# Optimization experiments

Hardware: AMD Instinct MI355X
Metric: run time of the kernel (lower is better)

Reference implementation:

```python
import jax, jax.numpy as jnp
import numpy as np

N = 50000
E = 800000
B = 8  # number of graphs


def gcn_conv(x, src, dst, W, b, n_nodes):
    # PyG GCNConv: add self-loops, symmetric deg^{-1/2} normalization,
    # linear transform, scatter-add aggregation at dst, then bias.
    loops = jnp.arange(n_nodes, dtype=src.dtype)
    s = jnp.concatenate([src, loops])
    d = jnp.concatenate([dst, loops])
    deg = jax.ops.segment_sum(jnp.ones_like(d, dtype=x.dtype), d, num_segments=n_nodes)
    dinv = jnp.where(deg > 0, jax.lax.rsqrt(deg), 0.0)
    norm = dinv[s] * dinv[d]                      # [E+N]
    xw = x @ W                                    # [N, out]
    msg = xw[s] * norm[:, None]                   # gather + scale
    out = jax.ops.segment_sum(msg, d, num_segments=n_nodes)  # scatter-add
    return out + b


def global_attention(x, batch, gate_w, gate_b, n_graphs):
    gate = x @ gate_w + gate_b                    # [N, 1]
    gmax = jax.ops.segment_max(gate, batch, num_segments=n_graphs)
    gmax = jnp.where(jnp.isfinite(gmax), gmax, 0.0)
    e = jnp.exp(gate - gmax[batch])               # segment-stable softmax
    denom = jax.ops.segment_sum(e, batch, num_segments=n_graphs)
    alpha = e / denom[batch]                      # [N, 1]
    return jax.ops.segment_sum(alpha * x, batch, num_segments=n_graphs)  # [B, d]


def setup_inputs() -> dict:
    key = jax.random.key(0)
    ks = jax.random.split(key, 10)
    x = jax.random.normal(ks[0], (N, 512), dtype=jnp.float32)
    edge_index = jax.random.randint(ks[1], (2, E), 0, N, dtype=jnp.int32)
    batch = jnp.sort(jax.random.randint(ks[2], (N,), 0, B, dtype=jnp.int32))
    W1 = jax.random.normal(ks[3], (512, 256), dtype=jnp.float32) / np.sqrt(512)
    b1 = jnp.zeros((256,), dtype=jnp.float32)
    W2 = jax.random.normal(ks[4], (256, 256), dtype=jnp.float32) / np.sqrt(256)
    b2 = jnp.zeros((256,), dtype=jnp.float32)
    gate_w = jax.random.normal(ks[5], (256, 1), dtype=jnp.float32) / np.sqrt(256)
    gate_b = jnp.zeros((1,), dtype=jnp.float32)
    return {"x": x, "edge_index": edge_index, "batch": batch,
            "W1": W1, "b1": b1, "W2": W2, "b2": b2,
            "gate_w": gate_w, "gate_b": gate_b}


def reference(x, edge_index, batch, W1, b1, W2, b2, gate_w, gate_b):
    src, dst = edge_index[0], edge_index[1]
    h = jax.nn.relu(gcn_conv(x, src, dst, W1, b1, N))
    h = jax.nn.relu(gcn_conv(h, src, dst, W2, b2, N))
    return global_attention(h, batch, gate_w, gate_b, B)
```

## Files before the change

kernel.cpp:

```cpp
#include <hip/hip_runtime.h>
#include <hip/hip_bf16.h>
#include <math.h>

#define FDIM 256
#define CAP 64
#define NGRAPH 8
#define GMAX_BLOCKS 64
#define FINAL_BLOCKS 512

typedef __attribute__((ext_vector_type(8))) short bf16x8;
typedef __attribute__((ext_vector_type(4))) float f32x4;

__device__ __forceinline__ unsigned enc_f(float x){
  unsigned u = __float_as_uint(x);
  return (u >> 31) ? ~u : (u | 0x80000000u);
}
__device__ __forceinline__ float dec_f(unsigned u){
  return (u >> 31) ? __uint_as_float(u & 0x7FFFFFFFu) : __uint_as_float(~u);
}

__device__ __forceinline__ unsigned short f2bf(float f){
  unsigned u = __float_as_uint(f);
  unsigned r = (u + 0x7FFFu + ((u >> 16) & 1u)) >> 16;
  return (unsigned short)r;
}
__device__ __forceinline__ float bf2f(unsigned short h){
  return __uint_as_float(((unsigned)h) << 16);
}
__device__ __forceinline__ unsigned pk2(float a, float b){
  return (unsigned)f2bf(a) | ((unsigned)f2bf(b) << 16);
}

__global__ void init_k(int* cnt, float* denom, float* out, int N){
  int i = blockIdx.x * blockDim.x + threadIdx.x;
  if (i < N) cnt[i] = 0;
  if (i < NGRAPH) denom[i] = 0.f;
  if (i < NGRAPH * FDIM) out[i] = 0.f;
}

__global__ void csr_k(const int* __restrict__ src, const int* __restrict__ dst,
                      int* __restrict__ cnt, int* __restrict__ col, int E){
  int e = blockIdx.x * blockDim.x + threadIdx.x;
  if (e < E){
    int d = dst[e];
    int pos = atomicAdd(&cnt[d], 1);
    if (pos < CAP) col[(size_t)d * CAP + pos] = src[e];
  }
}

__global__ void dinv_k(const int* __restrict__ cnt, float* __restrict__ dinv, int N){
  int i = blockIdx.x * blockDim.x + threadIdx.x;
  if (i < N) dinv[i] = rsqrtf((float)(cnt[i] + 1));
}

template<int K>
__global__ void wconv_k(const float* __restrict__ W, unsigned short* __restrict__ Wt){
  int idx = blockIdx.x * 256 + threadIdx.x;
  if (idx >= K * 256) return;
  int k = idx >> 8, n = idx & 255;
  Wt[(size_t)n * K + k] = f2bf(W[idx]);
}

template<int K, bool A_FP32>
__global__ __launch_bounds__(512) void gemm_k(const void* __restrict__ Av,
                                              const unsigned short* __restrict__ Bt,
                                              unsigned short* __restrict__ C, int M){
  __shared__ unsigned short As[128 * 64];
  __shared__ unsigned short Bs[256 * 64];
  const int tid = threadIdx.x;
  const int lane = tid & 63, wid = tid >> 6;
  const int wr = wid >> 2, wc = wid & 3;
  const int m0 = blockIdx.x * 128;
  f32x4 acc[4][4] = {};

  float4 arf0, arf1, arf2, arf3;
  uint4  arb0, arb1;
  uint4  brg0, brg1, brg2, brg3;

  const int rA0 = tid >> 3,          kqA0 = tid & 7;
  const int rA1 = (512 + tid) >> 3,  kqA1 = tid & 7;

  auto issue = [&](int k0){
    if (A_FP32){
      const float* A = (const float*)Av;
      const float* p0 = A + (size_t)min(m0 + rA0, M - 1) * K + k0 + kqA0 * 8;
      const float* p1 = A + (size_t)min(m0 + rA1, M - 1) * K + k0 + kqA1 * 8;
      arf0 = *(const float4*)p0; arf1 = *(const float4*)(p0 + 4);
      arf2 = *(const float4*)p1; arf3 = *(const float4*)(p1 + 4);
    } else {
      const unsigned short* A = (const unsigned short*)Av;
      arb0 = *(const uint4*)(A + (size_t)min(m0 + rA0, M - 1) * K + k0 + kqA0 * 8);
      arb1 = *(const uint4*)(A + (size_t)min(m0 + rA1, M - 1) * K + k0 + kqA1 * 8);
    }
    {
      int n0 = tid >> 3, n1 = (512 + tid) >> 3, n2 = (1024 + tid) >> 3, n3 = (1536 + tid) >> 3;
      int kq = tid & 7;
      brg0 = *(const uint4*)(Bt + (size_t)n0 * K + k0 + kq * 8);
      brg1 = *(const uint4*)(Bt + (size_t)n1 * K + k0 + kq * 8);
      brg2 = *(const uint4*)(Bt + (size_t)n2 * K + k0 + kq * 8);
      brg3 = *(const uint4*)(Bt + (size_t)n3 * K + k0 + kq * 8);
    }
  };

  auto writeLDS = [&](){
    int kq = tid & 7;
    {
      uint4 u0, u1;
      if (A_FP32){
        u0.x = pk2(arf0.x, arf0.y); u0.y = pk2(arf0.z, arf0.w);
        u0.z = pk2(arf1.x, arf1.y); u0.w = pk2(arf1.z, arf1.w);
        u1.x = pk2(arf2.x, arf2.y); u1.y = pk2(arf2.z, arf2.w);
        u1.z = pk2(arf3.x, arf3.y); u1.w = pk2(arf3.z, arf3.w);
      } else { u0 = arb0; u1 = arb1; }
      *(uint4*)((char*)As + ((rA0 * 128 + kq * 16) ^ ((rA0 & 7) << 4))) = u0;
      *(uint4*)((char*)As + ((rA1 * 128 + kq * 16) ^ ((rA1 & 7) << 4))) = u1;
    }
    {
      int n0 = tid >> 3, n1 = (512 + tid) >> 3, n2 = (1024 + tid) >> 3, n3 = (1536 + tid) >> 3;
      *(uint4*)((char*)Bs + ((n0 * 128 + kq * 16) ^ ((n0 & 7) << 4))) = brg0;
      *(uint4*)((char*)Bs + ((n1 * 128 + kq * 16) ^ ((n1 & 7) << 4))) = brg1;
      *(uint4*)((char*)Bs + ((n2 * 128 + kq * 16) ^ ((n2 & 7) << 4))) = brg2;
      *(uint4*)((char*)Bs + ((n3 * 128 + kq * 16) ^ ((n3 & 7) << 4))) = brg3;
    }
  };

  issue(0);
  for (int k0 = 0; k0 < K; k0 += 64){
    writeLDS();
    __syncthreads();
    if (k0 + 64 < K) issue(k0 + 64);

    #pragma unroll
    for (int kk = 0; kk < 64; kk += 32){
      bf16x8 af[4], bfr[4];
      int kb = kk * 2 + ((lane >> 4) << 4);
      #pragma unroll
      for (int mi = 0; mi < 4; ++mi){
        int r = wr * 64 + mi * 16 + (lane & 15);
        af[mi] = *(bf16x8*)((char*)As + ((r * 128 + kb) ^ ((r & 7) << 4)));
      }
      #pragma unroll
      for (int ni = 0; ni < 4; ++ni){
        int n = wc * 64 + ni * 16 + (lane & 15);
        bfr[ni] = *(bf16x8*)((char*)Bs + ((n * 128 + kb) ^ ((n & 7) << 4)));
      }
      #pragma unroll
      for (int mi = 0; mi < 4; ++mi)
        #pragma unroll
        for (int ni = 0; ni < 4; ++ni)
          acc[mi][ni] = __builtin_amdgcn_mfma_f32_16x16x32_bf16(af[mi], bfr[ni], acc[mi][ni], 0, 0, 0);
    }
    __syncthreads();
  }

  #pragma unroll
  for (int mi = 0; mi < 4; ++mi){
    #pragma unroll
    for (int reg = 0; reg < 4; ++reg){
      int row = m0 + wr * 64 + mi * 16 + ((lane >> 4) << 2) + reg;
      if (row < M){
        #pragma unroll
        for (int ni = 0; ni < 4; ++ni){
          int colc = wc * 64 + ni * 16 + (lane & 15);
          C[(size_t)row * FDIM + colc] = f2bf(acc[mi][ni][reg]);
        }
      }
    }
  }
}

template<bool OUT_BF16, bool GATE>
__global__ __launch_bounds__(64) void agg_k(const unsigned short* __restrict__ xw,
                                            const float* __restrict__ dinv,
                                            const int* __restrict__ col,
                                            const int* __restrict__ cnt,
                                            const float* __restrict__ bias,
                                            void* __restrict__ outv,
                                            const float* __restrict__ gw,
                                            const float* __restrict__ gb,
                                            float* __restrict__ gate, int N){
  int i = blockIdx.x;
  int lane = threadIdx.x;
  float di = dinv[i];
  int n = min(cnt[i], CAP);
  int s = 0; float w = 0.f;
  if (lane < n){ s = col[(size_t)i * CAP + lane]; w = di * dinv[s]; }

  float a0, a1, a2, a3;
  {
    ushort4 v = *(const ushort4*)(xw + (size_t)i * FDIM + lane * 4);
    float sw = di * di;
    a0 = sw * bf2f(v.x); a1 = sw * bf2f(v.y); a2 = sw * bf2f(v.z); a3 = sw * bf2f(v.w);
  }

  uint2 bufA[8], bufB[8];
  int nc = (n + 7) >> 3;

  auto loadChunk = [&](uint2 (&buf)[8], int c){
    #pragma unroll
    for (int j = 0; j < 8; ++j){
      int e = c * 8 + j;
      int se = __shfl(s, e);
      buf[j] = *(const uint2*)(xw + (size_t)se * FDIM + lane * 4);
    }
  };
  auto consChunk = [&](uint2 (&buf)[8], int c){
    #pragma unroll
    for (int j = 0; j < 8; ++j){
      int e = c * 8 + j;
      float we = __shfl(w, e);
      ushort4 v = *(ushort4*)&buf[j];
      a0 += we * bf2f(v.x); a1 += we * bf2f(v.y);
      a2 += we * bf2f(v.z); a3 += we * bf2f(v.w);
    }
  };

  if (nc > 0) loadChunk(bufA, 0);
  for (int c = 0; c < nc; ++c){
    if (c & 1){
      if (c + 1 < nc) loadChunk(bufA, c + 1);
      consChunk(bufB, c);
    } else {
      if (c + 1 < nc) loadChunk(bufB, c + 1);
      consChunk(bufA, c);
    }
  }

  float4 bv = *(const float4*)(bias + lane * 4);
  a0 = fmaxf(a0 + bv.x, 0.f); a1 = fmaxf(a1 + bv.y, 0.f);
  a2 = fmaxf(a2 + bv.z, 0.f); a3 = fmaxf(a3 + bv.w, 0.f);
  if (OUT_BF16){
    ushort4 r = make_ushort4(f2bf(a0), f2bf(a1), f2bf(a2), f2bf(a3));
    *(ushort4*)((unsigned short*)outv + (size_t)i * FDIM + lane * 4) = r;
  } else {
    *(float4*)((float*)outv + (size_t)i * FDIM + lane * 4) = make_float4(a0, a1, a2, a3);
  }
  if (GATE){
    float4 g = *(const float4*)(gw + lane * 4);
    float val = a0 * g.x + a1 * g.y + a2 * g.z + a3 * g.w;
    #pragma unroll
    for (int off = 32; off; off >>= 1) val += __shfl_down(val, off);
    if (lane == 0) gate[i] = val + gb[0];
  }
}

__global__ __launch_bounds__(256) void gmax_k(const float* __restrict__ gate,
                                              const int* __restrict__ batch,
                                              unsigned* __restrict__ pmax, int N){
  __shared__ unsigned smax[NGRAPH];
  int tid = threadIdx.x;
  if (tid < NGRAPH) smax[tid] = 0u;
  __syncthreads();
  int chunk = (N + gridDim.x - 1) / gridDim.x;
  int begin = blockIdx.x * chunk;
  int end = min(begin + chunk, N);
  int curg = -1; unsigned curm = 0u;
  for (int i = begin + tid; i < end; i += 256){
    int g = batch[i];
    unsigned v = enc_f(gate[i]);
    if (g != curg){
      if (curg >= 0) atomicMax(&smax[curg], curm);
      curg = g; curm = v;
    } else if (v > curm) curm = v;
  }
  if (curg >= 0) atomicMax(&smax[curg], curm);
  __syncthreads();
  if (tid < NGRAPH) pmax[blockIdx.x * NGRAPH + tid] = smax[tid];
}

__global__ __launch_bounds__(256) void denom_k(float* __restrict__ gate,
                                               const int* __restrict__ batch,
                                               const unsigned* __restrict__ pmax,
                                               float* __restrict__ denom, int N){
  __shared__ unsigned sge[NGRAPH];
  __shared__ float gm[NGRAPH];
  __shared__ float dsum[NGRAPH];
  int tid = threadIdx.x;
  if (tid < NGRAPH){ sge[tid] = 0u; dsum[tid] = 0.f; }
  __syncthreads();
  for (int j = tid; j < GMAX_BLOCKS * NGRAPH; j += 256)
    atomicMax(&sge[j & (NGRAPH - 1)], pmax[j]);
  __syncthreads();
  if (tid < NGRAPH){
    unsigned u = sge[tid];
    gm[tid] = (u == 0u) ? 0.f : dec_f(u);
  }
  __syncthreads();
  int chunk = (N + gridDim.x - 1) / gridDim.x;
  int begin = blockIdx.x * chunk;
  int end = min(begin + chunk, N);
  int curg = -1; float cursum = 0.f;
  for (int i = begin + tid; i < end; i += 256){
    int g = batch[i];
    float e = expf(gate[i] - gm[g]);
    gate[i] = e;
    if (g != curg){
      if (curg >= 0) atomicAdd(&dsum[curg], cursum);
      curg = g; cursum = e;
    } else cursum += e;
  }
  if (curg >= 0) atomicAdd(&dsum[curg], cursum);
  __syncthreads();
  if (tid < NGRAPH && dsum[tid] != 0.f) atomicAdd(&denom[tid], dsum[tid]);
}

__global__ __launch_bounds__(256) void final_k(const float* __restrict__ h,
                                               const float* __restrict__ e,
                                               const int* __restrict__ batch,
                                               const float* __restrict__ denom,
                                               float* __restrict__ out, int N){
  __shared__ float sacc[NGRAPH * FDIM];
  int tid = threadIdx.x;
  #pragma unroll
  for (int j = tid; j < NGRAPH * FDIM; j += 256) sacc[j] = 0.f;
  __syncthreads();
  int lane = tid & 63, w = tid >> 6;
  int chunk = (N + gridDim.x - 1) / gridDim.x;
  int begin = blockIdx.x * chunk;
  int end = min(begin + chunk, N);
  float4 acc = make_float4(0.f, 0.f, 0.f, 0.f);
  int curg = -1;
  for (int i = begin + w; i < end; i += 4){
    int g = batch[i];
    if (g != curg){
      if (curg >= 0){
        atomicAdd(&sacc[curg * FDIM + lane * 4 + 0], acc.x);
        atomicAdd(&sacc[curg * FDIM + lane * 4 + 1], acc.y);
        atomicAdd(&sacc[curg * FDIM + lane * 4 + 2], acc.z);
        atomicAdd(&sacc[curg * FDIM + lane * 4 + 3], acc.w);
        acc = make_float4(0.f, 0.f, 0.f, 0.f);
      }
      curg = g;
    }
    float alpha = e[i] / denom[g];
    float4 v = *(const float4*)(h + (size_t)i * FDIM + lane * 4);
    acc.x += alpha * v.x; acc.y += alpha * v.y;
    acc.z += alpha * v.z; acc.w += alpha * v.w;
  }
  if (curg >= 0){
    atomicAdd(&sacc[curg * FDIM + lane * 4 + 0], acc.x);
    atomicAdd(&sacc[curg * FDIM + lane * 4 + 1], acc.y);
    atomicAdd(&sacc[curg * FDIM + lane * 4 + 2], acc.z);
    atomicAdd(&sacc[curg * FDIM + lane * 4 + 3], acc.w);
  }
  __syncthreads();
  if (begin < end){
    int g0 = batch[begin], g1 = batch[end - 1];
    for (int g = g0; g <= g1; ++g){
      float v = sacc[g * FDIM + tid];
      if (v != 0.f) atomicAdd(&out[g * FDIM + tid], v);
    }
  }
}

extern "C" void kernel_launch(void* const* d_in, const int* in_sizes, int n_in,
                              void* d_out, int out_size, void* d_ws, size_t ws_size,
                              hipStream_t stream){
  const float* x     = (const float*)d_in[0];
  const int*   ei    = (const int*)  d_in[1];
  const int*   batch = (const int*)  d_in[2];
  const float* W1    = (const float*)d_in[3];
  const float* b1    = (const float*)d_in[4];
  const float* W2    = (const float*)d_in[5];
  const float* b2    = (const float*)d_in[6];
  const float* gw    = (const float*)d_in[7];
  const float* gb    = (const float*)d_in[8];
  float* out = (float*)d_out;

  const int N = in_sizes[2];
  const int E = in_sizes[1] / 2;
  const int* src = ei;
  const int* dst = ei + E;

  size_t off = 0;
  auto carve = [&](size_t bytes) -> void* {
    void* p = (char*)d_ws + off;
    off += (bytes + 255) / 256 * 256;
    return p;
  };
  float*          h     = (float*)         carve((size_t)N * FDIM * 4);
  unsigned short* h1b   = (unsigned short*)carve((size_t)N * FDIM * 2);
  unsigned short* xwb   = (unsigned short*)carve((size_t)N * FDIM * 2);
  int*            cnt   = (int*)           carve((size_t)N * 4);
  float*          dinv  = (float*)         carve((size_t)N * 4);
  int*            col   = (int*)           carve((size_t)N * CAP * 4);
  float*          gate  = (float*)         carve((size_t)N * 4);
  unsigned*       pmax  = (unsigned*)      carve(GMAX_BLOCKS * NGRAPH * 4);
  float*          denom = (float*)         carve(NGRAPH * 4);
  unsigned short* Wt1   = (unsigned short*)carve((size_t)256 * 512 * 2);
  unsigned short* Wt2   = (unsigned short*)carve((size_t)256 * 256 * 2);
  (void)ws_size; (void)n_in; (void)out_size;

  const int TB = 256;
  init_k<<<(N + TB - 1) / TB, TB, 0, stream>>>(cnt, denom, out, N);
  csr_k<<<(E + TB - 1) / TB, TB, 0, stream>>>(src, dst, cnt, col, E);
  dinv_k<<<(N + TB - 1) / TB, TB, 0, stream>>>(cnt, dinv, N);
  wconv_k<512><<<(512 * 256 + TB - 1) / TB, TB, 0, stream>>>(W1, Wt1);
  wconv_k<256><<<(256 * 256 + TB - 1) / TB, TB, 0, stream>>>(W2, Wt2);

  int gblocks = (N + 127) / 128;
  gemm_k<512, true ><<<gblocks, 512, 0, stream>>>(x,   Wt1, xwb, N);
  agg_k<true,  false><<<N, 64, 0, stream>>>(xwb, dinv, col, cnt, b1, h1b, nullptr, nullptr, nullptr, N);
  gemm_k<256, false><<<gblocks, 512, 0, stream>>>(h1b, Wt2, xwb, N);
  agg_k<false, true ><<<N, 64, 0, stream>>>(xwb, dinv, col, cnt, b2, h, gw, gb, gate, N);

  gmax_k<<<GMAX_BLOCKS, 256, 0, stream>>>(gate, batch, pmax, N);
  denom_k<<<GMAX_BLOCKS, 256, 0, stream>>>(gate, batch, pmax, denom, N);
  final_k<<<FINAL_BLOCKS, 256, 0, stream>>>(h, gate, batch, denom, out, N);
}
```

Baseline: 255.7 us.

## Pack four nodes per aggregation block, store final hidden as bf16, merge weight conversion

Measured after the change: 249.6 us. 1.02x faster.

```diff
diff --git a/kernel.cpp b/kernel.cpp
--- a/kernel.cpp
+++ b/kernel.cpp
@@ -53,12 +53,19 @@
   if (i < N) dinv[i] = rsqrtf((float)(cnt[i] + 1));
 }
 
-template<int K>
-__global__ void wconv_k(const float* __restrict__ W, unsigned short* __restrict__ Wt){
+__global__ void wconv_k(const float* __restrict__ W1, const float* __restrict__ W2,
+                        unsigned short* __restrict__ Wt1, unsigned short* __restrict__ Wt2){
   int idx = blockIdx.x * 256 + threadIdx.x;
-  if (idx >= K * 256) return;
-  int k = idx >> 8, n = idx & 255;
-  Wt[(size_t)n * K + k] = f2bf(W[idx]);
+  if (idx < 512 * 256){
+    int k = idx >> 8, n = idx & 255;
+    Wt1[(size_t)n * 512 + k] = f2bf(W1[idx]);
+  } else {
+    int j = idx - 512 * 256;
+    if (j < 256 * 256){
+      int k = j >> 8, n = j & 255;
+      Wt2[(size_t)n * 256 + k] = f2bf(W2[j]);
+    }
+  }
 }
 
 template<int K, bool A_FP32>
@@ -170,25 +177,26 @@
 }
 
 template<bool OUT_BF16, bool GATE>
-__global__ __launch_bounds__(64) void agg_k(const unsigned short* __restrict__ xw,
-                                            const float* __restrict__ dinv,
-                                            const int* __restrict__ col,
-                                            const int* __restrict__ cnt,
-                                            const float* __restrict__ bias,
-                                            void* __restrict__ outv,
-                                            const float* __restrict__ gw,
-                                            const float* __restrict__ gb,
-                                            float* __restrict__ gate, int N){
-  int i = blockIdx.x;
-  int lane = threadIdx.x;
-  float di = dinv[i];
-  int n = min(cnt[i], CAP);
+__global__ __launch_bounds__(256) void agg_k(const unsigned short* __restrict__ xw,
+                                             const float* __restrict__ dinv,
+                                             const int* __restrict__ col,
+                                             const int* __restrict__ cnt,
+                                             const float* __restrict__ bias,
+                                             void* __restrict__ outv,
+                                             const float* __restrict__ gw,
+                                             const float* __restrict__ gb,
+                                             float* __restrict__ gate, int N){
+  int node = blockIdx.x * 4 + (threadIdx.x >> 6);
+  if (node >= N) return;
+  int lane = threadIdx.x & 63;
+  float di = dinv[node];
+  int n = min(cnt[node], CAP);
   int s = 0; float w = 0.f;
-  if (lane < n){ s = col[(size_t)i * CAP + lane]; w = di * dinv[s]; }
+  if (lane < n){ s = col[(size_t)node * CAP + lane]; w = di * dinv[s]; }
 
   float a0, a1, a2, a3;
   {
-    ushort4 v = *(const ushort4*)(xw + (size_t)i * FDIM + lane * 4);
+    ushort4 v = *(const ushort4*)(xw + (size_t)node * FDIM + lane * 4);
     float sw = di * di;
     a0 = sw * bf2f(v.x); a1 = sw * bf2f(v.y); a2 = sw * bf2f(v.z); a3 = sw * bf2f(v.w);
   }
@@ -231,16 +239,16 @@
   a2 = fmaxf(a2 + bv.z, 0.f); a3 = fmaxf(a3 + bv.w, 0.f);
   if (OUT_BF16){
     ushort4 r = make_ushort4(f2bf(a0), f2bf(a1), f2bf(a2), f2bf(a3));
-    *(ushort4*)((unsigned short*)outv + (size_t)i * FDIM + lane * 4) = r;
+    *(ushort4*)((unsigned short*)outv + (size_t)node * FDIM + lane * 4) = r;
   } else {
-    *(float4*)((float*)outv + (size_t)i * FDIM + lane * 4) = make_float4(a0, a1, a2, a3);
+    *(float4*)((float*)outv + (size_t)node * FDIM + lane * 4) = make_float4(a0, a1, a2, a3);
   }
   if (GATE){
     float4 g = *(const float4*)(gw + lane * 4);
     float val = a0 * g.x + a1 * g.y + a2 * g.z + a3 * g.w;
     #pragma unroll
     for (int off = 32; off; off >>= 1) val += __shfl_down(val, off);
-    if (lane == 0) gate[i] = val + gb[0];
+    if (lane == 0) gate[node] = val + gb[0];
   }
 }
 
@@ -304,7 +312,7 @@
   if (tid < NGRAPH && dsum[tid] != 0.f) atomicAdd(&denom[tid], dsum[tid]);
 }
 
-__global__ __launch_bounds__(256) void final_k(const float* __restrict__ h,
+__global__ __launch_bounds__(256) void final_k(const unsigned short* __restrict__ h,
                                                const float* __restrict__ e,
                                                const int* __restrict__ batch,
                                                const float* __restrict__ denom,
@@ -333,9 +341,9 @@
       curg = g;
     }
     float alpha = e[i] / denom[g];
-    float4 v = *(const float4*)(h + (size_t)i * FDIM + lane * 4);
-    acc.x += alpha * v.x; acc.y += alpha * v.y;
-    acc.z += alpha * v.z; acc.w += alpha * v.w;
+    ushort4 v = *(const ushort4*)(h + (size_t)i * FDIM + lane * 4);
+    acc.x += alpha * bf2f(v.x); acc.y += alpha * bf2f(v.y);
+    acc.z += alpha * bf2f(v.z); acc.w += alpha * bf2f(v.w);
   }
   if (curg >= 0){
     atomicAdd(&sacc[curg * FDIM + lane * 4 + 0], acc.x);
@@ -378,7 +386,7 @@
     off += (bytes + 255) / 256 * 256;
     return p;
   };
-  float*          h     = (float*)         carve((size_t)N * FDIM * 4);
+  unsigned short* h     = (unsigned short*)carve((size_t)N * FDIM * 2);
   unsigned short* h1b   = (unsigned short*)carve((size_t)N * FDIM * 2);
   unsigned short* xwb   = (unsigned short*)carve((size_t)N * FDIM * 2);
   int*            cnt   = (int*)           carve((size_t)N * 4);
@@ -395,14 +403,14 @@
   init_k<<<(N + TB - 1) / TB, TB, 0, stream>>>(cnt, denom, out, N);
   csr_k<<<(E + TB - 1) / TB, TB, 0, stream>>>(src, dst, cnt, col, E);
   dinv_k<<<(N + TB - 1) / TB, TB, 0, stream>>>(cnt, dinv, N);
-  wconv_k<512><<<(512 * 256 + TB - 1) / TB, TB, 0, stream>>>(W1, Wt1);
-  wconv_k<256><<<(256 * 256 + TB - 1) / TB, TB, 0, stream>>>(W2, Wt2);
+  wconv_k<<<(512 * 256 + 256 * 256 + TB - 1) / TB, TB, 0, stream>>>(W1, W2, Wt1, Wt2);
 
   int gblocks = (N + 127) / 128;
+  int ablocks = (N + 3) / 4;
   gemm_k<512, true ><<<gblocks, 512, 0, stream>>>(x,   Wt1, xwb, N);
-  agg_k<true,  false><<<N, 64, 0, stream>>>(xwb, dinv, col, cnt, b1, h1b, nullptr, nullptr, nullptr, N);
+  agg_k<true,  false><<<ablocks, 256, 0, stream>>>(xwb, dinv, col, cnt, b1, h1b, nullptr, nullptr, nullptr, N);
   gemm_k<256, false><<<gblocks, 512, 0, stream>>>(h1b, Wt2, xwb, N);
-  agg_k<false, true ><<<N, 64, 0, stream>>>(xwb, dinv, col, cnt, b2, h, gw, gb, gate, N);
+  agg_k<true,  true ><<<ablocks, 256, 0, stream>>>(xwb, dinv, col, cnt, b2, h, gw, gb, gate, N);
 
   gmax_k<<<GMAX_BLOCKS, 256, 0, stream>>>(gate, batch, pmax, N);
   denom_k<<<GMAX_BLOCKS, 256, 0, stream>>>(gate, batch, pmax, denom, N);
```
